# Kernel tuning notes

Hardware: AMD Instinct MI355X
Metric: run time of the kernel (lower is better)

The kernel has to match this reference:

```python
import jax, jax.numpy as jnp
import numpy as np

B, E, D, H = 4096, 16, 512, 2048

def setup_inputs() -> dict:
    key = jax.random.key(0)
    k1, k2, k3, k4 = jax.random.split(key, 4)
    semantic_vec = jax.random.normal(k1, (B, D), dtype=jnp.float32)
    field_centers = jax.random.normal(k2, (E, D), dtype=jnp.float32)
    # Kaiming-uniform-ish Linear init scale
    lim = 1.0 / np.sqrt(D)
    W = jax.random.uniform(k3, (E, H, D), dtype=jnp.float32, minval=-lim, maxval=lim)
    b = jax.random.uniform(k4, (E, H), dtype=jnp.float32, minval=-lim, maxval=lim)
    return {"semantic_vec": semantic_vec, "field_centers": field_centers, "W": W, "b": b}

def reference(semantic_vec, field_centers, W, b):
    # Each expert e: relu((x - c_e) @ W_e^T + b_e); sum over experts.
    # Use linearity: (x - c_e) @ W_e^T = x @ W_e^T - c_e @ W_e^T, avoiding the [B,E,D] offsets tensor.
    xw = jnp.einsum('bd,ehd->beh', semantic_vec, W)          # [B,E,H]
    cw = jnp.einsum('ed,ehd->eh', field_centers, W)          # [E,H]
    pre = xw - cw[None, :, :] + b[None, :, :]                # [B,E,H]
    feature_anchor = jnp.sum(jax.nn.relu(pre), axis=1)       # [B,H]
    return feature_anchor
```

## Files before the change

### kernel.cpp

```cpp
#include <hip/hip_runtime.h>
#include <hip/hip_bf16.h>
#include <stdint.h>
#include <stddef.h>


#define B_DIM 4096
#define E_DIM 16
#define D_DIM 512
#define H_DIM 2048

typedef short bf16x8 __attribute__((ext_vector_type(8)));
typedef short bf16x4 __attribute__((ext_vector_type(4)));
typedef float f32x4 __attribute__((ext_vector_type(4)));

__device__ __forceinline__ short f2bf(float f) {
  __hip_bfloat16 h = __float2bfloat16(f);
  return *reinterpret_cast<short*>(&h);
}

__device__ __forceinline__ bf16x8 cvt8(float4 a, float4 b) {
  bf16x8 v;
  v[0] = f2bf(a.x); v[1] = f2bf(a.y); v[2] = f2bf(a.z); v[3] = f2bf(a.w);
  v[4] = f2bf(b.x); v[5] = f2bf(b.y); v[6] = f2bf(b.z); v[7] = f2bf(b.w);
  return v;
}

__device__ __forceinline__ bf16x4 cvt4(float4 a) {
  bf16x4 v;
  v[0] = f2bf(a.x); v[1] = f2bf(a.y); v[2] = f2bf(a.z); v[3] = f2bf(a.w);
  return v;
}

__device__ __forceinline__ float dot4(float4 a, float4 b) {
  return a.x * b.x + a.y * b.y + a.z * b.z + a.w * b.w;
}

__device__ __forceinline__ void async_copy16(const void* gptr, void* lptr) {
  __builtin_amdgcn_global_load_lds(
      (const __attribute__((address_space(1))) void*)gptr,
      (__attribute__((address_space(3))) void*)lptr,
      16, 0, 0);
}

__global__ __launch_bounds__(256) void prep(
    const float* __restrict__ W, const float* __restrict__ C,
    const float* __restrict__ bias, const float* __restrict__ X,
    __hip_bfloat16* __restrict__ Wb, float* __restrict__ bias2,
    __hip_bfloat16* __restrict__ Xb) {
  if (blockIdx.x < 4096) {
    const int wid = (blockIdx.x * 256 + threadIdx.x) >> 6;
    const int lane = threadIdx.x & 63;
    const int e = wid >> 10;
    const size_t base = (size_t)wid * 1024 + lane * 4;

    const float4 cA = *(const float4*)(C + e * D_DIM + lane * 4);
    const float4 cB = *(const float4*)(C + e * D_DIM + 256 + lane * 4);

    float4 w0 = *(const float4*)(W + base);
    float4 w1 = *(const float4*)(W + base + 256);
    float4 w2 = *(const float4*)(W + base + 512);
    float4 w3 = *(const float4*)(W + base + 768);

    *(bf16x4*)(Wb + base) = cvt4(w0);
    *(bf16x4*)(Wb + base + 256) = cvt4(w1);
    *(bf16x4*)(Wb + base + 512) = cvt4(w2);
    *(bf16x4*)(Wb + base + 768) = cvt4(w3);

    float dot0 = dot4(w0, cA) + dot4(w1, cB);
    float dot1 = dot4(w2, cA) + dot4(w3, cB);
#pragma unroll
    for (int off = 32; off > 0; off >>= 1) {
      dot0 += __shfl_down(dot0, off, 64);
      dot1 += __shfl_down(dot1, off, 64);
    }
    if (lane == 0) {
      bias2[2 * wid] = bias[2 * wid] - dot0;
      bias2[2 * wid + 1] = bias[2 * wid + 1] - dot1;
    }
  } else {
    const size_t t = (size_t)(blockIdx.x - 4096) * 256 + threadIdx.x;
    const size_t i0 = t * 4;
    const size_t i1 = i0 + (size_t)262144 * 4;
    float4 a0 = *(const float4*)(X + i0);
    float4 a1 = *(const float4*)(X + i1);
    *(bf16x4*)(Xb + i0) = cvt4(a0);
    *(bf16x4*)(Xb + i1) = cvt4(a1);
  }
}

__global__ __launch_bounds__(256, 4) void moe_gemm(
    const __hip_bfloat16* __restrict__ Xb,
    const __hip_bfloat16* __restrict__ Wb,
    const float* __restrict__ bias2,
    float* __restrict__ out) {
  __shared__ __align__(16) __hip_bfloat16 As[2][128 * 32];
  __shared__ __align__(16) __hip_bfloat16 Bs[2][2][64 * 32];
  __shared__ __align__(16) float biasS[E_DIM * 64];

  const int tid = threadIdx.x;
  const int lane = tid & 63;
  const int wave = tid >> 6;
  const int hi = blockIdx.x & 31;
  const int mi = blockIdx.x >> 5;
  const int m0 = mi * 128;
  const int h0 = hi * 64;

  for (int idx = tid; idx < E_DIM * 64; idx += 256) {
    biasS[idx] = bias2[((idx >> 6) << 11) + h0 + (idx & 63)];
  }

  const int wm = (wave & 1) * 64;
  const int wn = (wave >> 1) * 32;
  const int lm = lane & 15;
  const int q = lane >> 4;

  const int r = tid >> 2;
  const int fr = (r >> 1) & 3;
  const int col = (((tid & 3) ^ fr)) << 3;
  const size_t aOff0 = (size_t)(m0 + r) * D_DIM + col;
  const size_t aOff1 = (size_t)(m0 + r + 64) * D_DIM + col;
  const size_t bOff = (size_t)(h0 + r) * D_DIM + col;
  const int ldA0 = tid * 8;
  const int ldA1 = (tid + 256) * 8;
  const int ldB = tid * 8;

  int offA[4], offB[2];
#pragma unroll
  for (int i = 0; i < 4; ++i) {
    const int R = wm + i * 16 + lm;
    offA[i] = R * 32 + ((q ^ ((R >> 1) & 3)) << 3);
  }
#pragma unroll
  for (int j = 0; j < 2; ++j) {
    const int R = wn + j * 16 + lm;
    offB[j] = R * 32 + ((q ^ ((R >> 1) & 3)) << 3);
  }

  f32x4 sum[4][2], acc0[4][2], acc1[4][2];
#pragma unroll
  for (int i = 0; i < 4; ++i)
#pragma unroll
    for (int j = 0; j < 2; ++j) {
      sum[i][j] = (f32x4){0.f, 0.f, 0.f, 0.f};
      acc0[i][j] = (f32x4){0.f, 0.f, 0.f, 0.f};
      acc1[i][j] = (f32x4){0.f, 0.f, 0.f, 0.f};
    }

#define STAGE(buf, tt)                                                      \
  {                                                                         \
    const int kk = ((tt) & 15) << 5;                                        \
    const __hip_bfloat16* Bb = Wb + ((size_t)((tt) >> 4) << 21) + bOff + kk;\
    async_copy16(Xb + aOff0 + kk, &As[buf][ldA0]);                          \
    async_copy16(Xb + aOff1 + kk, &As[buf][ldA1]);                          \
    async_copy16(Bb, &Bs[buf][0][ldB]);                                     \
    async_copy16(Bb + ((size_t)1 << 20), &Bs[buf][1][ldB]);                 \
  }

  STAGE(0, 0);
  __syncthreads();

  for (int t = 0; t < 128; ++t) {
    const int cur = t & 1;
    if (t < 127) STAGE(cur ^ 1, t + 1);

    bf16x8 af[4];
#pragma unroll
    for (int i = 0; i < 4; ++i) af[i] = *(const bf16x8*)&As[cur][offA[i]];

#pragma unroll
    for (int j = 0; j < 2; ++j) {
      const bf16x8 b0 = *(const bf16x8*)&Bs[cur][0][offB[j]];
#pragma unroll
      for (int i = 0; i < 4; ++i)
        acc0[i][j] = __builtin_amdgcn_mfma_f32_16x16x32_bf16(
            af[i], b0, acc0[i][j], 0, 0, 0);
      const bf16x8 b1 = *(const bf16x8*)&Bs[cur][1][offB[j]];
#pragma unroll
      for (int i = 0; i < 4; ++i)
        acc1[i][j] = __builtin_amdgcn_mfma_f32_16x16x32_bf16(
            af[i], b1, acc1[i][j], 0, 0, 0);
    }

    if ((t & 15) == 15) {
      const int pair = t >> 4;
#pragma unroll
      for (int j = 0; j < 2; ++j) {
        const float bv0 = biasS[(2 * pair) * 64 + wn + j * 16 + lm];
        const float bv1 = biasS[(2 * pair + 1) * 64 + wn + j * 16 + lm];
#pragma unroll
        for (int i = 0; i < 4; ++i)
#pragma unroll
          for (int u = 0; u < 4; ++u) {
            sum[i][j][u] += fmaxf(acc0[i][j][u] + bv0, 0.f) +
                            fmaxf(acc1[i][j][u] + bv1, 0.f);
            acc0[i][j][u] = 0.f;
            acc1[i][j][u] = 0.f;
          }
      }
    }

    __syncthreads();
  }
#undef STAGE

  const int rbase = q * 4;
#pragma unroll
  for (int i = 0; i < 4; ++i)
#pragma unroll
    for (int j = 0; j < 2; ++j)
#pragma unroll
      for (int u = 0; u < 4; ++u)
        out[(size_t)(m0 + wm + i * 16 + rbase + u) * H_DIM + h0 + wn + j * 16 + lm] =
            sum[i][j][u];
}

__global__ __launch_bounds__(256) void naive_kernel(
    const float* __restrict__ x, const float* __restrict__ c,
    const float* __restrict__ W, const float* __restrict__ bias,
    float* __restrict__ out) {
  const int idx = blockIdx.x * 256 + threadIdx.x;
  const int b = idx >> 11;
  const int h = idx & (H_DIM - 1);
  const float* xr = x + (size_t)b * D_DIM;
  float s = 0.f;
  for (int e = 0; e < E_DIM; ++e) {
    const float* wr = W + ((size_t)e * H_DIM + h) * D_DIM;
    const float* cr = c + (size_t)e * D_DIM;
    float acc = bias[e * H_DIM + h];
    for (int d = 0; d < D_DIM; ++d) acc += (xr[d] - cr[d]) * wr[d];
    s += fmaxf(acc, 0.f);
  }
  out[idx] = s;
}

extern "C" void kernel_launch(void* const* d_in, const int* in_sizes, int n_in,
                              void* d_out, int out_size, void* d_ws, size_t ws_size,
                              hipStream_t stream) {
  const float* x = (const float*)d_in[0];
  const float* c = (const float*)d_in[1];
  const float* W = (const float*)d_in[2];
  const float* b = (const float*)d_in[3];
  float* out = (float*)d_out;

  const size_t sz_wb = (size_t)E_DIM * H_DIM * D_DIM * 2;
  const size_t sz_xb = (size_t)B_DIM * D_DIM * 2;
  const size_t sz_b2 = (size_t)E_DIM * H_DIM * 4;
  const size_t need = sz_wb + sz_xb + sz_b2;

  if (ws_size >= need) {
    __hip_bfloat16* Wb = (__hip_bfloat16*)((char*)d_ws);
    __hip_bfloat16* Xb = (__hip_bfloat16*)((char*)d_ws + sz_wb);
    float* bias2 = (float*)((char*)d_ws + sz_wb + sz_xb);
    prep<<<5120, 256, 0, stream>>>(W, c, b, x, Wb, bias2, Xb);
    moe_gemm<<<1024, 256, 0, stream>>>(Xb, Wb, bias2, out);
  } else {
    naive_kernel<<<(B_DIM * H_DIM) / 256, 256, 0, stream>>>(x, c, W, b, out);
  }
}
```

Before: 265.8 us.

## Fuse prep and GEMM into one cooperative kernel with grid sync

Merges the bf16 conversion and bias-folding prep pass into the GEMM kernel, launched cooperatively with 1024 blocks and a grid-wide barrier between the two phases. The aim is to drop one kernel launch and the gap between kernels, and to let converted data still sit in L2 when the GEMM reads it. The cost is a grid sync, restricted prep parallelism (4 rows per wave in a loop), and a dependence on the occupancy check reporting that 4 blocks per CU fit so that all 1024 blocks are co-resident.

```diff
diff --git a/kernel.cpp b/kernel.cpp
--- a/kernel.cpp
+++ b/kernel.cpp
@@ -1,8 +1,11 @@
 #include <hip/hip_runtime.h>
 #include <hip/hip_bf16.h>
+#include <hip/hip_cooperative_groups.h>
 #include <stdint.h>
 #include <stddef.h>
 
+
+namespace cg = cooperative_groups;
 
 #define B_DIM 4096
 #define E_DIM 16
@@ -16,13 +19,6 @@
 __device__ __forceinline__ short f2bf(float f) {
   __hip_bfloat16 h = __float2bfloat16(f);
   return *reinterpret_cast<short*>(&h);
-}
-
-__device__ __forceinline__ bf16x8 cvt8(float4 a, float4 b) {
-  bf16x8 v;
-  v[0] = f2bf(a.x); v[1] = f2bf(a.y); v[2] = f2bf(a.z); v[3] = f2bf(a.w);
-  v[4] = f2bf(b.x); v[5] = f2bf(b.y); v[6] = f2bf(b.z); v[7] = f2bf(b.w);
-  return v;
 }
 
 __device__ __forceinline__ bf16x4 cvt4(float4 a) {
@@ -40,6 +36,177 @@
       (const __attribute__((address_space(1))) void*)gptr,
       (__attribute__((address_space(3))) void*)lptr,
       16, 0, 0);
+}
+
+__global__ __launch_bounds__(256, 4) void fused(
+    const float* __restrict__ X, const float* __restrict__ C,
+    const float* __restrict__ W, const float* __restrict__ bias,
+    __hip_bfloat16* Wb, float* bias2, __hip_bfloat16* Xb,
+    float* __restrict__ out) {
+  __shared__ __align__(16) __hip_bfloat16 As[2][128 * 32];
+  __shared__ __align__(16) __hip_bfloat16 Bs[2][2][64 * 32];
+  __shared__ __align__(16) float biasS[E_DIM * 64];
+
+  const int tid = threadIdx.x;
+  const int bid = blockIdx.x;
+  const int lane = tid & 63;
+  const int wave = tid >> 6;
+
+  {
+    const size_t tt = (size_t)bid * 256 + tid;
+    const size_t i0 = tt * 8;
+    float4 a0 = *(const float4*)(X + i0);
+    float4 a1 = *(const float4*)(X + i0 + 4);
+    *(bf16x4*)(Xb + i0) = cvt4(a0);
+    *(bf16x4*)(Xb + i0 + 4) = cvt4(a1);
+
+    const int gw = (bid << 2) + wave;
+    for (int it = 0; it < 4; ++it) {
+      const int wid = (gw << 2) + it;
+      const int e = wid >> 10;
+      const size_t base = (size_t)wid * 1024 + lane * 4;
+
+      const float4 cA = *(const float4*)(C + e * D_DIM + lane * 4);
+      const float4 cB = *(const float4*)(C + e * D_DIM + 256 + lane * 4);
+
+      float4 w0 = *(const float4*)(W + base);
+      float4 w1 = *(const float4*)(W + base + 256);
+      float4 w2 = *(const float4*)(W + base + 512);
+      float4 w3 = *(const float4*)(W + base + 768);
+
+      *(bf16x4*)(Wb + base) = cvt4(w0);
+      *(bf16x4*)(Wb + base + 256) = cvt4(w1);
+      *(bf16x4*)(Wb + base + 512) = cvt4(w2);
+      *(bf16x4*)(Wb + base + 768) = cvt4(w3);
+
+      float dot0 = dot4(w0, cA) + dot4(w1, cB);
+      float dot1 = dot4(w2, cA) + dot4(w3, cB);
+#pragma unroll
+      for (int off = 32; off > 0; off >>= 1) {
+        dot0 += __shfl_down(dot0, off, 64);
+        dot1 += __shfl_down(dot1, off, 64);
+      }
+      if (lane == 0) {
+        bias2[2 * wid] = bias[2 * wid] - dot0;
+        bias2[2 * wid + 1] = bias[2 * wid + 1] - dot1;
+      }
+    }
+  }
+
+  cg::this_grid().sync();
+
+  const int hi = bid & 31;
+  const int mi = bid >> 5;
+  const int m0 = mi * 128;
+  const int h0 = hi * 64;
+
+  for (int idx = tid; idx < E_DIM * 64; idx += 256) {
+    biasS[idx] = bias2[((idx >> 6) << 11) + h0 + (idx & 63)];
+  }
+
+  const int wm = (wave & 1) * 64;
+  const int wn = (wave >> 1) * 32;
+  const int lm = lane & 15;
+  const int q = lane >> 4;
+
+  const int r = tid >> 2;
+  const int fr = (r >> 1) & 3;
+  const int col = (((tid & 3) ^ fr)) << 3;
+  const size_t aOff0 = (size_t)(m0 + r) * D_DIM + col;
+  const size_t aOff1 = (size_t)(m0 + r + 64) * D_DIM + col;
+  const size_t bOff = (size_t)(h0 + r) * D_DIM + col;
+  const int ldA0 = tid * 8;
+  const int ldA1 = (tid + 256) * 8;
+  const int ldB = tid * 8;
+
+  int offA[4], offB[2];
+#pragma unroll
+  for (int i = 0; i < 4; ++i) {
+    const int R = wm + i * 16 + lm;
+    offA[i] = R * 32 + ((q ^ ((R >> 1) & 3)) << 3);
+  }
+#pragma unroll
+  for (int j = 0; j < 2; ++j) {
+    const int R = wn + j * 16 + lm;
+    offB[j] = R * 32 + ((q ^ ((R >> 1) & 3)) << 3);
+  }
+
+  f32x4 sum[4][2], acc0[4][2], acc1[4][2];
+#pragma unroll
+  for (int i = 0; i < 4; ++i)
+#pragma unroll
+    for (int j = 0; j < 2; ++j) {
+      sum[i][j] = (f32x4){0.f, 0.f, 0.f, 0.f};
+      acc0[i][j] = (f32x4){0.f, 0.f, 0.f, 0.f};
+      acc1[i][j] = (f32x4){0.f, 0.f, 0.f, 0.f};
+    }
+
+#define STAGE(buf, tt)                                                      \
+  {                                                                         \
+    const int kk = ((tt) & 15) << 5;                                        \
+    const __hip_bfloat16* Bb = Wb + ((size_t)((tt) >> 4) << 21) + bOff + kk;\
+    async_copy16(Xb + aOff0 + kk, &As[buf][ldA0]);                          \
+    async_copy16(Xb + aOff1 + kk, &As[buf][ldA1]);                          \
+    async_copy16(Bb, &Bs[buf][0][ldB]);                                     \
+    async_copy16(Bb + ((size_t)1 << 20), &Bs[buf][1][ldB]);                 \
+  }
+
+  STAGE(0, 0);
+  __syncthreads();
+
+  for (int t = 0; t < 128; ++t) {
+    const int cur = t & 1;
+    if (t < 127) STAGE(cur ^ 1, t + 1);
+
+    bf16x8 af[4];
+#pragma unroll
+    for (int i = 0; i < 4; ++i) af[i] = *(const bf16x8*)&As[cur][offA[i]];
+
+#pragma unroll
+    for (int j = 0; j < 2; ++j) {
+      const bf16x8 b0 = *(const bf16x8*)&Bs[cur][0][offB[j]];
+#pragma unroll
+      for (int i = 0; i < 4; ++i)
+        acc0[i][j] = __builtin_amdgcn_mfma_f32_16x16x32_bf16(
+            af[i], b0, acc0[i][j], 0, 0, 0);
+      const bf16x8 b1 = *(const bf16x8*)&Bs[cur][1][offB[j]];
+#pragma unroll
+      for (int i = 0; i < 4; ++i)
+        acc1[i][j] = __builtin_amdgcn_mfma_f32_16x16x32_bf16(
+            af[i], b1, acc1[i][j], 0, 0, 0);
+    }
+
+    if ((t & 15) == 15) {
+      const int pair = t >> 4;
+#pragma unroll
+      for (int j = 0; j < 2; ++j) {
+        const float bv0 = biasS[(2 * pair) * 64 + wn + j * 16 + lm];
+        const float bv1 = biasS[(2 * pair + 1) * 64 + wn + j * 16 + lm];
+#pragma unroll
+        for (int i = 0; i < 4; ++i)
+#pragma unroll
+          for (int u = 0; u < 4; ++u) {
+            sum[i][j][u] += fmaxf(acc0[i][j][u] + bv0, 0.f) +
+                            fmaxf(acc1[i][j][u] + bv1, 0.f);
+            acc0[i][j][u] = 0.f;
+            acc1[i][j][u] = 0.f;
+          }
+      }
+    }
+
+    __syncthreads();
+  }
+#undef STAGE
+
+  const int rbase = q * 4;
+#pragma unroll
+  for (int i = 0; i < 4; ++i)
+#pragma unroll
+    for (int j = 0; j < 2; ++j)
+#pragma unroll
+      for (int u = 0; u < 4; ++u)
+        out[(size_t)(m0 + wm + i * 16 + rbase + u) * H_DIM + h0 + wn + j * 16 + lm] =
+            sum[i][j][u];
 }
 
 __global__ __launch_bounds__(256) void prep(
@@ -52,20 +219,16 @@
     const int lane = threadIdx.x & 63;
     const int e = wid >> 10;
     const size_t base = (size_t)wid * 1024 + lane * 4;
-
     const float4 cA = *(const float4*)(C + e * D_DIM + lane * 4);
     const float4 cB = *(const float4*)(C + e * D_DIM + 256 + lane * 4);
-
     float4 w0 = *(const float4*)(W + base);
     float4 w1 = *(const float4*)(W + base + 256);
     float4 w2 = *(const float4*)(W + base + 512);
     float4 w3 = *(const float4*)(W + base + 768);
-
     *(bf16x4*)(Wb + base) = cvt4(w0);
     *(bf16x4*)(Wb + base + 256) = cvt4(w1);
     *(bf16x4*)(Wb + base + 512) = cvt4(w2);
     *(bf16x4*)(Wb + base + 768) = cvt4(w3);
-
     float dot0 = dot4(w0, cA) + dot4(w1, cB);
     float dot1 = dot4(w2, cA) + dot4(w3, cB);
 #pragma unroll
@@ -89,10 +252,8 @@
 }
 
 __global__ __launch_bounds__(256, 4) void moe_gemm(
-    const __hip_bfloat16* __restrict__ Xb,
-    const __hip_bfloat16* __restrict__ Wb,
-    const float* __restrict__ bias2,
-    float* __restrict__ out) {
+    const __hip_bfloat16* __restrict__ Xb, const __hip_bfloat16* __restrict__ Wb,
+    const float* __restrict__ bias2, float* __restrict__ out) {
   __shared__ __align__(16) __hip_bfloat16 As[2][128 * 32];
   __shared__ __align__(16) __hip_bfloat16 Bs[2][2][64 * 32];
   __shared__ __align__(16) float biasS[E_DIM * 64];
@@ -251,8 +412,23 @@
     __hip_bfloat16* Wb = (__hip_bfloat16*)((char*)d_ws);
     __hip_bfloat16* Xb = (__hip_bfloat16*)((char*)d_ws + sz_wb);
     float* bias2 = (float*)((char*)d_ws + sz_wb + sz_xb);
-    prep<<<5120, 256, 0, stream>>>(W, c, b, x, Wb, bias2, Xb);
-    moe_gemm<<<1024, 256, 0, stream>>>(Xb, Wb, bias2, out);
+
+    static int coop_ok = -1;
+    if (coop_ok < 0) {
+      int nb = 0;
+      hipError_t e =
+          hipOccupancyMaxActiveBlocksPerMultiprocessor(&nb, fused, 256, 0);
+      coop_ok = (e == hipSuccess && nb >= 4) ? 1 : 0;
+    }
+
+    if (coop_ok) {
+      void* args[] = {(void*)&x, (void*)&c, (void*)&W, (void*)&b,
+                      (void*)&Wb, (void*)&bias2, (void*)&Xb, (void*)&out};
+      hipLaunchCooperativeKernel(fused, dim3(1024), dim3(256), args, 0, stream);
+    } else {
+      prep<<<5120, 256, 0, stream>>>(W, c, b, x, Wb, bias2, Xb);
+      moe_gemm<<<1024, 256, 0, stream>>>(Xb, Wb, bias2, out);
+    }
   } else {
     naive_kernel<<<(B_DIM * H_DIM) / 256, 256, 0, stream>>>(x, c, W, b, out);
   }
```

New measurement: 262.3 us. About the same (-1.3%).

## Add 256x128-tile triple-buffered MFMA GEMM with block swizzle and manual waitcnt

Applied to the files above, without the earlier changes.

Adds a new GEMM kernel with 512 threads and a 256x128 output tile. It loads 64-wide K slices into a three-stage LDS ring of about 152 KB, using manual vmcnt waits and a single barrier per step. An XOR swizzle avoids LDS bank conflicts, an XCD-aware block remap improves L2 reuse, and setprio is raised around the MFMA bursts. The larger tile increases reuse of each loaded operand and cuts the number of blocks from 1024 to 256. The costs are heavy LDS use, which limits occupancy, and a single wave of 256 blocks on a 256-CU device. A runtime occupancy check falls back to the old kernel.

```diff
diff --git a/kernel.cpp b/kernel.cpp
--- a/kernel.cpp
+++ b/kernel.cpp
@@ -16,13 +16,6 @@
 __device__ __forceinline__ short f2bf(float f) {
   __hip_bfloat16 h = __float2bfloat16(f);
   return *reinterpret_cast<short*>(&h);
-}
-
-__device__ __forceinline__ bf16x8 cvt8(float4 a, float4 b) {
-  bf16x8 v;
-  v[0] = f2bf(a.x); v[1] = f2bf(a.y); v[2] = f2bf(a.z); v[3] = f2bf(a.w);
-  v[4] = f2bf(b.x); v[5] = f2bf(b.y); v[6] = f2bf(b.z); v[7] = f2bf(b.w);
-  return v;
 }
 
 __device__ __forceinline__ bf16x4 cvt4(float4 a) {
@@ -52,20 +45,16 @@
     const int lane = threadIdx.x & 63;
     const int e = wid >> 10;
     const size_t base = (size_t)wid * 1024 + lane * 4;
-
     const float4 cA = *(const float4*)(C + e * D_DIM + lane * 4);
     const float4 cB = *(const float4*)(C + e * D_DIM + 256 + lane * 4);
-
     float4 w0 = *(const float4*)(W + base);
     float4 w1 = *(const float4*)(W + base + 256);
     float4 w2 = *(const float4*)(W + base + 512);
     float4 w3 = *(const float4*)(W + base + 768);
-
     *(bf16x4*)(Wb + base) = cvt4(w0);
     *(bf16x4*)(Wb + base + 256) = cvt4(w1);
     *(bf16x4*)(Wb + base + 512) = cvt4(w2);
     *(bf16x4*)(Wb + base + 768) = cvt4(w3);
-
     float dot0 = dot4(w0, cA) + dot4(w1, cB);
     float dot1 = dot4(w2, cA) + dot4(w3, cB);
 #pragma unroll
@@ -88,11 +77,165 @@
   }
 }
 
-__global__ __launch_bounds__(256, 4) void moe_gemm(
+__global__ __launch_bounds__(512, 2) void moe_gemm8(
     const __hip_bfloat16* __restrict__ Xb,
     const __hip_bfloat16* __restrict__ Wb,
     const float* __restrict__ bias2,
     float* __restrict__ out) {
+  __shared__ __align__(16) char smem[155648];
+
+  const int tid = threadIdx.x;
+  const int lane = tid & 63;
+  const int wave = tid >> 6;
+
+  const int swz = (blockIdx.x & 7) * 32 + (blockIdx.x >> 3);
+  const int mi = swz >> 4;
+  const int hi = swz & 15;
+  const int m0 = mi * 256;
+  const int h0 = hi * 128;
+
+  const int wm = (wave >> 1) * 64;
+  const int wn = (wave & 1) * 64;
+  const int lm = lane & 15;
+  const int q = lane >> 4;
+
+  int aSrc[4], bSrc[2];
+#pragma unroll
+  for (int j = 0; j < 4; ++j) {
+    const int n = j * 512 + tid;
+    const int r = n >> 3;
+    const int c = (n & 7) ^ (r & 7);
+    aSrc[j] = r * D_DIM + c * 8;
+  }
+#pragma unroll
+  for (int j = 0; j < 2; ++j) {
+    const int n = j * 512 + tid;
+    const int r = n >> 3;
+    const int c = (n & 7) ^ (r & 7);
+    bSrc[j] = r * D_DIM + c * 8;
+  }
+
+  int aRd[4][2], bRd[4][2];
+#pragma unroll
+  for (int m = 0; m < 4; ++m) {
+    const int R = wm + m * 16 + lm;
+#pragma unroll
+    for (int s = 0; s < 2; ++s)
+      aRd[m][s] = R * 128 + (((s * 4 + q) ^ (R & 7)) << 4);
+  }
+#pragma unroll
+  for (int n = 0; n < 4; ++n) {
+    const int R = wn + n * 16 + lm;
+#pragma unroll
+    for (int s = 0; s < 2; ++s)
+      bRd[n][s] = 32768 + R * 128 + (((s * 4 + q) ^ (R & 7)) << 4);
+  }
+
+#define STAGE8(bufOff, gg)                                                   \
+  {                                                                          \
+    const int eS = (gg) >> 3;                                                \
+    const int k0 = ((gg) & 7) << 6;                                          \
+    const __hip_bfloat16* Ag = Xb + (size_t)m0 * D_DIM + k0;                 \
+    const __hip_bfloat16* Bg =                                               \
+        Wb + ((size_t)eS << 20) + (size_t)h0 * D_DIM + k0;                   \
+    _Pragma("unroll")                                                        \
+    for (int j = 0; j < 4; ++j)                                              \
+      async_copy16(Ag + aSrc[j], smem + (bufOff) + (j * 512 + tid) * 16);    \
+    _Pragma("unroll")                                                        \
+    for (int j = 0; j < 2; ++j)                                              \
+      async_copy16(Bg + bSrc[j],                                             \
+                   smem + (bufOff) + 32768 + (j * 512 + tid) * 16);          \
+  }
+
+  STAGE8(0, 0);
+  STAGE8(49152, 1);
+  {
+    float* bS = (float*)(smem + 147456);
+#pragma unroll
+    for (int j = 0; j < 4; ++j) {
+      const int idx = j * 512 + tid;
+      bS[idx] = bias2[((idx >> 7) << 11) + h0 + (idx & 127)];
+    }
+  }
+  asm volatile("s_waitcnt vmcnt(6) lgkmcnt(0)" ::: "memory");
+  __builtin_amdgcn_s_barrier();
+  __builtin_amdgcn_sched_barrier(0);
+
+  f32x4 sum[4][4], acc[4][4];
+#pragma unroll
+  for (int m = 0; m < 4; ++m)
+#pragma unroll
+    for (int n = 0; n < 4; ++n) {
+      sum[m][n] = (f32x4){0.f, 0.f, 0.f, 0.f};
+      acc[m][n] = (f32x4){0.f, 0.f, 0.f, 0.f};
+    }
+
+  int bC = 0, bN = 49152, bS2 = 98304;
+
+  for (int g = 0; g < 128; ++g) {
+    if (g < 126) STAGE8(bS2, g + 2);
+
+#pragma unroll
+    for (int s = 0; s < 2; ++s) {
+      bf16x8 aF[4], bF[4];
+#pragma unroll
+      for (int m = 0; m < 4; ++m)
+        aF[m] = *(const bf16x8*)(smem + bC + aRd[m][s]);
+#pragma unroll
+      for (int n = 0; n < 4; ++n)
+        bF[n] = *(const bf16x8*)(smem + bC + bRd[n][s]);
+      asm volatile("s_waitcnt lgkmcnt(0)" ::: "memory");
+      __builtin_amdgcn_sched_barrier(0);
+      __builtin_amdgcn_s_setprio(1);
+#pragma unroll
+      for (int m = 0; m < 4; ++m)
+#pragma unroll
+        for (int n = 0; n < 4; ++n)
+          acc[m][n] = __builtin_amdgcn_mfma_f32_16x16x32_bf16(
+              aF[m], bF[n], acc[m][n], 0, 0, 0);
+      __builtin_amdgcn_s_setprio(0);
+    }
+
+    if ((g & 7) == 7) {
+      const float* bv =
+          (const float*)(smem + 147456) + ((g >> 3) << 7) + wn + lm;
+#pragma unroll
+      for (int n = 0; n < 4; ++n) {
+        const float bvn = bv[n * 16];
+#pragma unroll
+        for (int m = 0; m < 4; ++m)
+#pragma unroll
+          for (int u = 0; u < 4; ++u) {
+            sum[m][n][u] += fmaxf(acc[m][n][u] + bvn, 0.f);
+            acc[m][n][u] = 0.f;
+          }
+      }
+    }
+
+    if (g < 126)
+      asm volatile("s_waitcnt vmcnt(6)" ::: "memory");
+    else
+      asm volatile("s_waitcnt vmcnt(0)" ::: "memory");
+    __builtin_amdgcn_s_barrier();
+    __builtin_amdgcn_sched_barrier(0);
+
+    const int t_ = bC; bC = bN; bN = bS2; bS2 = t_;
+  }
+#undef STAGE8
+
+#pragma unroll
+  for (int m = 0; m < 4; ++m)
+#pragma unroll
+    for (int n = 0; n < 4; ++n)
+#pragma unroll
+      for (int u = 0; u < 4; ++u)
+        out[(size_t)(m0 + wm + m * 16 + q * 4 + u) * H_DIM +
+            h0 + wn + n * 16 + lm] = sum[m][n][u];
+}
+
+__global__ __launch_bounds__(256, 4) void moe_gemm(
+    const __hip_bfloat16* __restrict__ Xb, const __hip_bfloat16* __restrict__ Wb,
+    const float* __restrict__ bias2, float* __restrict__ out) {
   __shared__ __align__(16) __hip_bfloat16 As[2][128 * 32];
   __shared__ __align__(16) __hip_bfloat16 Bs[2][2][64 * 32];
   __shared__ __align__(16) float biasS[E_DIM * 64];
@@ -251,8 +394,21 @@
     __hip_bfloat16* Wb = (__hip_bfloat16*)((char*)d_ws);
     __hip_bfloat16* Xb = (__hip_bfloat16*)((char*)d_ws + sz_wb);
     float* bias2 = (float*)((char*)d_ws + sz_wb + sz_xb);
+
+    static int g8_ok = -1;
+    if (g8_ok < 0) {
+      int nb = 0;
+      hipError_t e =
+          hipOccupancyMaxActiveBlocksPerMultiprocessor(&nb, moe_gemm8, 512, 0);
+      g8_ok = (e == hipSuccess && nb >= 1) ? 1 : 0;
+    }
+
     prep<<<5120, 256, 0, stream>>>(W, c, b, x, Wb, bias2, Xb);
-    moe_gemm<<<1024, 256, 0, stream>>>(Xb, Wb, bias2, out);
+    if (g8_ok) {
+      moe_gemm8<<<256, 512, 0, stream>>>(Xb, Wb, bias2, out);
+    } else {
+      moe_gemm<<<1024, 256, 0, stream>>>(Xb, Wb, bias2, out);
+    }
   } else {
     naive_kernel<<<(B_DIM * H_DIM) / 256, 256, 0, stream>>>(x, c, W, b, out);
   }
```

Result: no change. 262.2 us (-1.4%).
